# Performance work log

Measured on AMD Instinct MI355X. Metric: run time of the kernel, lower is better.

## Reference

```python
import jax, jax.numpy as jnp
import numpy as np
from jax import lax

LN_EPS = 1e-5

def _layer_norm(x, g, b):
    mu = jnp.mean(x, axis=-1, keepdims=True)
    var = jnp.mean(jnp.square(x - mu), axis=-1, keepdims=True)
    return (x - mu) * lax.rsqrt(var + LN_EPS) * g + b

def _conv1d_same(x, w, b):
    # x: [B, T, Cin], w: [K, Cin, Cout] (kernel=3, padding=1 == SAME)
    y = lax.conv_general_dilated(x, w, window_strides=(1,), padding='SAME',
                                 dimension_numbers=('NWC', 'WIO', 'NWC'))
    return y + b

def setup_inputs() -> dict:
    key = jax.random.key(0)
    ks = jax.random.split(key, 8)
    B, T_enc, D, F = 16, 512, 256, 256
    x = jax.random.normal(ks[0], (B, T_enc, D), dtype=jnp.float32)
    target = jax.random.randint(ks[1], (B, T_enc), 0, 8).astype(jnp.int32)
    s = 0.05
    w1 = jax.random.normal(ks[2], (3, D, F), dtype=jnp.float32) * s
    w2 = jax.random.normal(ks[3], (3, F, F), dtype=jnp.float32) * s
    wl = jax.random.normal(ks[4], (F, 1), dtype=jnp.float32) * s
    return {
        'x': x, 'target': target,
        'w1': w1, 'b1': jnp.zeros((F,), jnp.float32),
        'g1': jnp.ones((F,), jnp.float32), 'be1': jnp.zeros((F,), jnp.float32),
        'w2': w2, 'b2': jnp.zeros((F,), jnp.float32),
        'g2': jnp.ones((F,), jnp.float32), 'be2': jnp.zeros((F,), jnp.float32),
        'wl': wl, 'bl': jnp.zeros((1,), jnp.float32),
        'mel_max_length': 4096,
    }

def reference(x, target, w1, b1, g1, be1, w2, b2, g2, be2, wl, bl, mel_max_length):
    # --- DurationPredictor (eval mode, dropout off) ---
    h = jax.nn.relu(_layer_norm(_conv1d_same(x, w1, b1), g1, be1))
    h = jax.nn.relu(_layer_norm(_conv1d_same(h, w2, b2), g2, be2))
    duration_predictor_output = jnp.exp(h @ wl + bl)[..., 0]  # [B, T_enc]
    # --- LR with ground-truth target durations (training branch) ---
    # alignment[b, t, j] = 1 iff cumsum(target)[b, j-1] <= t < cumsum(target)[b, j]
    cum = jnp.cumsum(target, axis=1)                      # [B, T_enc]
    t = jnp.arange(mel_max_length, dtype=target.dtype)    # [T_mel]
    temp = cum[:, None, :] - t[None, :, None]             # [B, T_mel, T_enc]
    pos = temp > 0
    cond2 = (target[:, None, :] - jnp.where(pos, temp, 0)) >= 0
    alignment = (pos & cond2).astype(x.dtype)             # rows past sum are all-zero => built-in padding
    output = jnp.einsum('bme,bed->bmd', alignment, x)     # [B, T_mel, D]
    return output, alignment, duration_predictor_output
```

## Files before the change

### kernel.cpp

```cpp
#include <hip/hip_runtime.h>

typedef __attribute__((ext_vector_type(8))) short short8;
typedef __attribute__((ext_vector_type(4))) float f32x4;

#define NB   16
#define TENC 512
#define DCH  256
#define TMEL 4096
#define ROWS (NB*TENC)

__device__ __forceinline__ unsigned short f2bf(float f){
  unsigned u = __builtin_bit_cast(unsigned, f);
  u += 0x7FFFu + ((u >> 16) & 1u);
  return (unsigned short)(u >> 16);
}

__global__ __launch_bounds__(256) void prep_scan_kernel(
    const float* __restrict__ x, const int* __restrict__ target,
    const float* __restrict__ w1, const float* __restrict__ w2,
    unsigned* __restrict__ xb32,
    unsigned short* __restrict__ w1p, unsigned short* __restrict__ w2p,
    int* __restrict__ cum, int* __restrict__ total, int* __restrict__ src){
  __shared__ int wsum[4];
  __shared__ int stot;
  int bid = blockIdx.x, tid = threadIdx.x;
  if (bid < 16){
    int lane = tid & 63, wv = tid >> 6;
    int a0 = target[bid * 512 + 2 * tid];
    int a1 = target[bid * 512 + 2 * tid + 1];
    int ps = a0 + a1;
    #pragma unroll
    for (int off = 1; off < 64; off <<= 1){
      int v = __shfl_up(ps, off);
      if (lane >= off) ps += v;
    }
    if (lane == 63) wsum[wv] = ps;
    __syncthreads();
    int add = 0;
    #pragma unroll
    for (int w = 0; w < 4; ++w){ int s = wsum[w]; if (w < wv) add += s; }
    ps += add;
    int c1 = ps;
    int c0 = ps - a1;
    int cp = c0 - a0;
    cum[bid * 512 + 2 * tid]     = c0;
    cum[bid * 512 + 2 * tid + 1] = c1;
    if (tid == 255){ total[bid] = c1; stot = c1; }
    int* sb = src + bid * TMEL;
    for (int t = cp; t < c0; ++t) sb[t] = 2 * tid;
    for (int t = c0; t < c1; ++t) sb[t] = 2 * tid + 1;
    __syncthreads();
    for (int t = stot + tid; t < TMEL; t += 256) sb[t] = -1;
  } else if (bid < 16 + 2048){
    int i = (bid - 16) * 256 + tid;
    const f32x4 v = *reinterpret_cast<const f32x4*>(x + 4 * (size_t)i);
    unsigned lo = (unsigned)f2bf(v.x) | ((unsigned)f2bf(v.y) << 16);
    unsigned hi = (unsigned)f2bf(v.z) | ((unsigned)f2bf(v.w) << 16);
    xb32[2 * i]     = lo;
    xb32[2 * i + 1] = hi;
  } else {
    int i = (bid - 16 - 2048) * 256 + tid;
    int j = i & 7, lane = (i >> 3) & 63, nt = (i >> 9) & 15, ks = i >> 13;
    int r   = ks * 32 + ((lane >> 4) * 8) + j;
    int col = nt * 16 + (lane & 15);
    w1p[i] = f2bf(w1[r * 256 + col]);
    w2p[i] = f2bf(w2[r * 256 + col]);
  }
}

__global__ __launch_bounds__(256, 4) void fused_kernel(
    const float* __restrict__ x, const int* __restrict__ src,
    const unsigned short* __restrict__ xb,
    const unsigned short* __restrict__ w1p, const unsigned short* __restrict__ w2p,
    const float* __restrict__ b1, const float* __restrict__ g1, const float* __restrict__ be1,
    const float* __restrict__ b2, const float* __restrict__ g2, const float* __restrict__ be2,
    const float* __restrict__ wl, const float* __restrict__ bl,
    float* __restrict__ out0, float* __restrict__ alignp, float* __restrict__ durp)
{
  __shared__ unsigned short hsw[48 * 256];
  __shared__ float red[48][4][2];
  __shared__ float dred[16][4];
  int tid = threadIdx.x;

  if (blockIdx.x >= 512){
    int row  = (blockIdx.x - 512) * 4 + (tid >> 6);
    int lane = tid & 63;
    int b = row >> 12;
    int s = __builtin_amdgcn_readfirstlane(src[row]);
    size_t orow = (size_t)row * 256;
    size_t arow = (size_t)row * 512;
    f32x4 z = {0.f, 0.f, 0.f, 0.f};
    if (s < 0){
      *reinterpret_cast<f32x4*>(out0 + orow + lane * 4) = z;
      *reinterpret_cast<f32x4*>(alignp + arow + lane * 8) = z;
      *reinterpret_cast<f32x4*>(alignp + arow + lane * 8 + 4) = z;
      return;
    }
    const f32x4 v = *reinterpret_cast<const f32x4*>(x + ((size_t)b * TENC + s) * DCH + lane * 4);
    *reinterpret_cast<f32x4*>(out0 + orow + lane * 4) = v;
    f32x4 a0 = z, a1 = z;
    int rel = s - lane * 8;
    if (rel >= 0 && rel < 8){
      if (rel < 4) a0[rel] = 1.0f; else a1[rel - 4] = 1.0f;
    }
    *reinterpret_cast<f32x4*>(alignp + arow + lane * 8) = a0;
    *reinterpret_cast<f32x4*>(alignp + arow + lane * 8 + 4) = a1;
    return;
  }

  int m0 = blockIdx.x * 16;
  int rowlo = (m0 >> 9) << 9, rowhi = rowlo + 512;
  int wave = tid >> 6, l = tid & 63, kgrp = l >> 4, l16 = l & 15;
  int colb = wave * 64 + l16;

  f32x4 acc[3][4];
  #pragma unroll
  for (int mt = 0; mt < 3; ++mt)
    #pragma unroll
    for (int nt = 0; nt < 4; ++nt) acc[mt][nt] = (f32x4)0.0f;

  for (int ks = 0; ks < 24; ++ks){
    int shift = ks >> 3;
    int c = (ks & 7) * 32 + kgrp * 8;
    const unsigned short* wb = w1p + (size_t)(ks * 16 + wave * 4) * 512 + l * 8;
    short8 bf0 = *reinterpret_cast<const short8*>(wb);
    short8 bf1 = *reinterpret_cast<const short8*>(wb + 512);
    short8 bf2 = *reinterpret_cast<const short8*>(wb + 1024);
    short8 bf3 = *reinterpret_cast<const short8*>(wb + 1536);
    #pragma unroll
    for (int mt = 0; mt < 3; ++mt){
      int grow = m0 - 16 + mt * 16 + l16 + shift - 1;
      short8 a = {0,0,0,0,0,0,0,0};
      if (grow >= rowlo && grow < rowhi)
        a = *reinterpret_cast<const short8*>(xb + (size_t)grow * 256 + c);
      acc[mt][0] = __builtin_amdgcn_mfma_f32_16x16x32_bf16(a, bf0, acc[mt][0], 0, 0, 0);
      acc[mt][1] = __builtin_amdgcn_mfma_f32_16x16x32_bf16(a, bf1, acc[mt][1], 0, 0, 0);
      acc[mt][2] = __builtin_amdgcn_mfma_f32_16x16x32_bf16(a, bf2, acc[mt][2], 0, 0, 0);
      acc[mt][3] = __builtin_amdgcn_mfma_f32_16x16x32_bf16(a, bf3, acc[mt][3], 0, 0, 0);
    }
  }
  #pragma unroll
  for (int mt = 0; mt < 3; ++mt){
    float s1[4] = {0,0,0,0}, s2[4] = {0,0,0,0};
    #pragma unroll
    for (int nt = 0; nt < 4; ++nt){
      float bv = b1[colb + nt * 16];
      #pragma unroll
      for (int q = 0; q < 4; ++q){
        float v = acc[mt][nt][q] + bv;
        acc[mt][nt][q] = v;
        s1[q] += v; s2[q] += v * v;
      }
    }
    #pragma unroll
    for (int m = 1; m < 16; m <<= 1)
      #pragma unroll
      for (int q = 0; q < 4; ++q){
        s1[q] += __shfl_xor(s1[q], m);
        s2[q] += __shfl_xor(s2[q], m);
      }
    if (l16 == 0)
      #pragma unroll
      for (int q = 0; q < 4; ++q){
        red[mt * 16 + kgrp * 4 + q][wave][0] = s1[q];
        red[mt * 16 + kgrp * 4 + q][wave][1] = s2[q];
      }
  }
  __syncthreads();
  float mu[3][4], rs[3][4];
  #pragma unroll
  for (int mt = 0; mt < 3; ++mt)
    #pragma unroll
    for (int q = 0; q < 4; ++q){
      int r = mt * 16 + kgrp * 4 + q;
      float S1 = red[r][0][0] + red[r][1][0] + red[r][2][0] + red[r][3][0];
      float S2 = red[r][0][1] + red[r][1][1] + red[r][2][1] + red[r][3][1];
      float m_ = S1 * (1.0f / 256.0f);
      float var = S2 * (1.0f / 256.0f) - m_ * m_;
      mu[mt][q] = m_;
      rs[mt][q] = rsqrtf(var + 1e-5f);
    }
  #pragma unroll
  for (int mt = 0; mt < 3; ++mt)
    #pragma unroll
    for (int nt = 0; nt < 4; ++nt){
      int col = colb + nt * 16;
      float g = g1[col], be = be1[col];
      #pragma unroll
      for (int q = 0; q < 4; ++q){
        int r = mt * 16 + kgrp * 4 + q;
        int gq = m0 - 16 + r;
        float y = fmaxf((acc[mt][nt][q] - mu[mt][q]) * rs[mt][q] * g + be, 0.0f);
        unsigned short hv = (gq >= rowlo && gq < rowhi) ? f2bf(y) : (unsigned short)0;
        hsw[r * 256 + (col ^ ((r & 7) << 3))] = hv;
      }
    }
  __syncthreads();

  f32x4 acc2[4];
  #pragma unroll
  for (int nt = 0; nt < 4; ++nt) acc2[nt] = (f32x4)0.0f;

  for (int ks = 0; ks < 24; ++ks){
    int shift = ks >> 3;
    int c = (ks & 7) * 32 + kgrp * 8;
    const unsigned short* wb = w2p + (size_t)(ks * 16 + wave * 4) * 512 + l * 8;
    short8 bf0 = *reinterpret_cast<const short8*>(wb);
    short8 bf1 = *reinterpret_cast<const short8*>(wb + 512);
    short8 bf2 = *reinterpret_cast<const short8*>(wb + 1024);
    short8 bf3 = *reinterpret_cast<const short8*>(wb + 1536);
    int rr = 16 + l16 + shift - 1;
    short8 a = *reinterpret_cast<const short8*>(hsw + rr * 256 + (c ^ ((rr & 7) << 3)));
    acc2[0] = __builtin_amdgcn_mfma_f32_16x16x32_bf16(a, bf0, acc2[0], 0, 0, 0);
    acc2[1] = __builtin_amdgcn_mfma_f32_16x16x32_bf16(a, bf1, acc2[1], 0, 0, 0);
    acc2[2] = __builtin_amdgcn_mfma_f32_16x16x32_bf16(a, bf2, acc2[2], 0, 0, 0);
    acc2[3] = __builtin_amdgcn_mfma_f32_16x16x32_bf16(a, bf3, acc2[3], 0, 0, 0);
  }
  __syncthreads();
  {
    float s1[4] = {0,0,0,0}, s2[4] = {0,0,0,0};
    #pragma unroll
    for (int nt = 0; nt < 4; ++nt){
      float bv = b2[colb + nt * 16];
      #pragma unroll
      for (int q = 0; q < 4; ++q){
        float v = acc2[nt][q] + bv;
        acc2[nt][q] = v;
        s1[q] += v; s2[q] += v * v;
      }
    }
    #pragma unroll
    for (int m = 1; m < 16; m <<= 1)
      #pragma unroll
      for (int q = 0; q < 4; ++q){
        s1[q] += __shfl_xor(s1[q], m);
        s2[q] += __shfl_xor(s2[q], m);
      }
    if (l16 == 0)
      #pragma unroll
      for (int q = 0; q < 4; ++q){
        red[kgrp * 4 + q][wave][0] = s1[q];
        red[kgrp * 4 + q][wave][1] = s2[q];
      }
  }
  __syncthreads();
  {
    float mu2[4], rs2[4];
    #pragma unroll
    for (int q = 0; q < 4; ++q){
      int r = kgrp * 4 + q;
      float S1 = red[r][0][0] + red[r][1][0] + red[r][2][0] + red[r][3][0];
      float S2 = red[r][0][1] + red[r][1][1] + red[r][2][1] + red[r][3][1];
      float m_ = S1 * (1.0f / 256.0f);
      float var = S2 * (1.0f / 256.0f) - m_ * m_;
      mu2[q] = m_;
      rs2[q] = rsqrtf(var + 1e-5f);
    }
    float dp[4] = {0,0,0,0};
    #pragma unroll
    for (int nt = 0; nt < 4; ++nt){
      int col = colb + nt * 16;
      float g = g2[col], be = be2[col], wv = wl[col];
      #pragma unroll
      for (int q = 0; q < 4; ++q){
        float y = fmaxf((acc2[nt][q] - mu2[q]) * rs2[q] * g + be, 0.0f);
        dp[q] += y * wv;
      }
    }
    #pragma unroll
    for (int m = 1; m < 16; m <<= 1)
      #pragma unroll
      for (int q = 0; q < 4; ++q) dp[q] += __shfl_xor(dp[q], m);
    if (l16 == 0)
      #pragma unroll
      for (int q = 0; q < 4; ++q) dred[kgrp * 4 + q][wave] = dp[q];
  }
  __syncthreads();
  if (tid < 16)
    durp[m0 + tid] = expf(dred[tid][0] + dred[tid][1] + dred[tid][2] + dred[tid][3] + bl[0]);
}

extern "C" void kernel_launch(void* const* d_in, const int* in_sizes, int n_in,
                              void* d_out, int out_size, void* d_ws, size_t ws_size,
                              hipStream_t stream){
  const float* x   = (const float*)d_in[0];
  const int*   target = (const int*)d_in[1];
  const float* w1  = (const float*)d_in[2];
  const float* b1  = (const float*)d_in[3];
  const float* g1  = (const float*)d_in[4];
  const float* be1 = (const float*)d_in[5];
  const float* w2  = (const float*)d_in[6];
  const float* b2  = (const float*)d_in[7];
  const float* g2  = (const float*)d_in[8];
  const float* be2 = (const float*)d_in[9];
  const float* wl  = (const float*)d_in[10];
  const float* bl  = (const float*)d_in[11];

  float* out0   = (float*)d_out;
  float* alignp = out0 + (size_t)NB * TMEL * DCH;
  float* durp   = alignp + (size_t)NB * TMEL * TENC;

  char* ws = (char*)d_ws;
  int* cum   = (int*)ws;
  int* total = (int*)(ws + 32768);
  int* src   = (int*)(ws + 65536);
  unsigned short* xb  = (unsigned short*)(ws + 65536 + 262144);
  unsigned short* w1p = (unsigned short*)(ws + 65536 + 262144 + 4194304);
  unsigned short* w2p = (unsigned short*)(ws + 65536 + 262144 + 4194304 + 393216);

  prep_scan_kernel<<<2832, 256, 0, stream>>>(x, target, w1, w2,
      (unsigned*)xb, w1p, w2p, cum, total, src);
  fused_kernel<<<512 + NB * TMEL / 4, 256, 0, stream>>>(x, src, xb, w1p, w2p,
      b1, g1, be1, b2, g2, be2, wl, bl, out0, alignp, durp);
}
```

Measured before the change: 65.05 us.

## Fuse x bf16 conversion into conv kernel via swizzled LDS halo tile

```diff
diff --git a/kernel.cpp b/kernel.cpp
--- a/kernel.cpp
+++ b/kernel.cpp
@@ -2,6 +2,7 @@
 
 typedef __attribute__((ext_vector_type(8))) short short8;
 typedef __attribute__((ext_vector_type(4))) float f32x4;
+typedef __attribute__((ext_vector_type(2))) unsigned u32x2;
 
 #define NB   16
 #define TENC 512
@@ -16,11 +17,10 @@
 }
 
 __global__ __launch_bounds__(256) void prep_scan_kernel(
-    const float* __restrict__ x, const int* __restrict__ target,
+    const int* __restrict__ target,
     const float* __restrict__ w1, const float* __restrict__ w2,
-    unsigned* __restrict__ xb32,
     unsigned short* __restrict__ w1p, unsigned short* __restrict__ w2p,
-    int* __restrict__ cum, int* __restrict__ total, int* __restrict__ src){
+    int* __restrict__ src){
   __shared__ int wsum[4];
   __shared__ int stot;
   int bid = blockIdx.x, tid = threadIdx.x;
@@ -43,42 +43,34 @@
     int c1 = ps;
     int c0 = ps - a1;
     int cp = c0 - a0;
-    cum[bid * 512 + 2 * tid]     = c0;
-    cum[bid * 512 + 2 * tid + 1] = c1;
-    if (tid == 255){ total[bid] = c1; stot = c1; }
+    if (tid == 255) stot = c1;
     int* sb = src + bid * TMEL;
     for (int t = cp; t < c0; ++t) sb[t] = 2 * tid;
     for (int t = c0; t < c1; ++t) sb[t] = 2 * tid + 1;
     __syncthreads();
     for (int t = stot + tid; t < TMEL; t += 256) sb[t] = -1;
-  } else if (bid < 16 + 2048){
+  } else {
     int i = (bid - 16) * 256 + tid;
-    const f32x4 v = *reinterpret_cast<const f32x4*>(x + 4 * (size_t)i);
-    unsigned lo = (unsigned)f2bf(v.x) | ((unsigned)f2bf(v.y) << 16);
-    unsigned hi = (unsigned)f2bf(v.z) | ((unsigned)f2bf(v.w) << 16);
-    xb32[2 * i]     = lo;
-    xb32[2 * i + 1] = hi;
-  } else {
-    int i = (bid - 16 - 2048) * 256 + tid;
-    int j = i & 7, lane = (i >> 3) & 63, nt = (i >> 9) & 15, ks = i >> 13;
-    int r   = ks * 32 + ((lane >> 4) * 8) + j;
-    int col = nt * 16 + (lane & 15);
-    w1p[i] = f2bf(w1[r * 256 + col]);
-    w2p[i] = f2bf(w2[r * 256 + col]);
+    int r = i >> 8, col = i & 255;
+    int ks = r >> 5, rh = (r >> 3) & 3, j = r & 7;
+    int nt = col >> 4, lane = rh * 16 + (col & 15);
+    int o = (((ks << 4) + nt) << 9) + (lane << 3) + j;
+    w1p[o] = f2bf(w1[i]);
+    w2p[o] = f2bf(w2[i]);
   }
 }
 
 __global__ __launch_bounds__(256, 4) void fused_kernel(
     const float* __restrict__ x, const int* __restrict__ src,
-    const unsigned short* __restrict__ xb,
     const unsigned short* __restrict__ w1p, const unsigned short* __restrict__ w2p,
     const float* __restrict__ b1, const float* __restrict__ g1, const float* __restrict__ be1,
     const float* __restrict__ b2, const float* __restrict__ g2, const float* __restrict__ be2,
     const float* __restrict__ wl, const float* __restrict__ bl,
     float* __restrict__ out0, float* __restrict__ alignp, float* __restrict__ durp)
 {
-  __shared__ unsigned short hsw[48 * 256];
-  __shared__ float red[48][4][2];
+  __shared__ unsigned short xsw[34 * 256];
+  __shared__ unsigned short hsw[32 * 256];
+  __shared__ float red[32][4][2];
   __shared__ float dred[16][4];
   int tid = threadIdx.x;
 
@@ -113,9 +105,29 @@
   int wave = tid >> 6, l = tid & 63, kgrp = l >> 4, l16 = l & 15;
   int colb = wave * 64 + l16;
 
-  f32x4 acc[3][4];
-  #pragma unroll
-  for (int mt = 0; mt < 3; ++mt)
+  {
+    int lane = l;
+    #pragma unroll
+    for (int it = 0; it < 9; ++it){
+      int rr = it * 4 + wave;
+      if (rr < 34){
+        int grow = m0 - 2 + rr;
+        f32x4 v = {0.f, 0.f, 0.f, 0.f};
+        if (grow >= rowlo && grow < rowhi)
+          v = *reinterpret_cast<const f32x4*>(x + (size_t)grow * 256 + lane * 4);
+        unsigned lo = (unsigned)f2bf(v.x) | ((unsigned)f2bf(v.y) << 16);
+        unsigned hi = (unsigned)f2bf(v.z) | ((unsigned)f2bf(v.w) << 16);
+        int col = lane * 4;
+        u32x2 pk = {lo, hi};
+        *reinterpret_cast<u32x2*>(xsw + rr * 256 + (col ^ ((rr & 7) << 3))) = pk;
+      }
+    }
+  }
+  __syncthreads();
+
+  f32x4 acc[2][4];
+  #pragma unroll
+  for (int mt = 0; mt < 2; ++mt)
     #pragma unroll
     for (int nt = 0; nt < 4; ++nt) acc[mt][nt] = (f32x4)0.0f;
 
@@ -128,11 +140,9 @@
     short8 bf2 = *reinterpret_cast<const short8*>(wb + 1024);
     short8 bf3 = *reinterpret_cast<const short8*>(wb + 1536);
     #pragma unroll
-    for (int mt = 0; mt < 3; ++mt){
-      int grow = m0 - 16 + mt * 16 + l16 + shift - 1;
-      short8 a = {0,0,0,0,0,0,0,0};
-      if (grow >= rowlo && grow < rowhi)
-        a = *reinterpret_cast<const short8*>(xb + (size_t)grow * 256 + c);
+    for (int mt = 0; mt < 2; ++mt){
+      int rr = mt * 16 + l16 + shift;
+      short8 a = *reinterpret_cast<const short8*>(xsw + rr * 256 + (c ^ ((rr & 7) << 3)));
       acc[mt][0] = __builtin_amdgcn_mfma_f32_16x16x32_bf16(a, bf0, acc[mt][0], 0, 0, 0);
       acc[mt][1] = __builtin_amdgcn_mfma_f32_16x16x32_bf16(a, bf1, acc[mt][1], 0, 0, 0);
       acc[mt][2] = __builtin_amdgcn_mfma_f32_16x16x32_bf16(a, bf2, acc[mt][2], 0, 0, 0);
@@ -140,7 +150,7 @@
     }
   }
   #pragma unroll
-  for (int mt = 0; mt < 3; ++mt){
+  for (int mt = 0; mt < 2; ++mt){
     float s1[4] = {0,0,0,0}, s2[4] = {0,0,0,0};
     #pragma unroll
     for (int nt = 0; nt < 4; ++nt){
@@ -167,9 +177,9 @@
       }
   }
   __syncthreads();
-  float mu[3][4], rs[3][4];
-  #pragma unroll
-  for (int mt = 0; mt < 3; ++mt)
+  float mu[2][4], rs[2][4];
+  #pragma unroll
+  for (int mt = 0; mt < 2; ++mt)
     #pragma unroll
     for (int q = 0; q < 4; ++q){
       int r = mt * 16 + kgrp * 4 + q;
@@ -181,7 +191,7 @@
       rs[mt][q] = rsqrtf(var + 1e-5f);
     }
   #pragma unroll
-  for (int mt = 0; mt < 3; ++mt)
+  for (int mt = 0; mt < 2; ++mt)
     #pragma unroll
     for (int nt = 0; nt < 4; ++nt){
       int col = colb + nt * 16;
@@ -189,7 +199,7 @@
       #pragma unroll
       for (int q = 0; q < 4; ++q){
         int r = mt * 16 + kgrp * 4 + q;
-        int gq = m0 - 16 + r;
+        int gq = m0 - 1 + r;
         float y = fmaxf((acc[mt][nt][q] - mu[mt][q]) * rs[mt][q] * g + be, 0.0f);
         unsigned short hv = (gq >= rowlo && gq < rowhi) ? f2bf(y) : (unsigned short)0;
         hsw[r * 256 + (col ^ ((r & 7) << 3))] = hv;
@@ -209,7 +219,7 @@
     short8 bf1 = *reinterpret_cast<const short8*>(wb + 512);
     short8 bf2 = *reinterpret_cast<const short8*>(wb + 1024);
     short8 bf3 = *reinterpret_cast<const short8*>(wb + 1536);
-    int rr = 16 + l16 + shift - 1;
+    int rr = l16 + shift;
     short8 a = *reinterpret_cast<const short8*>(hsw + rr * 256 + (c ^ ((rr & 7) << 3)));
     acc2[0] = __builtin_amdgcn_mfma_f32_16x16x32_bf16(a, bf0, acc2[0], 0, 0, 0);
     acc2[1] = __builtin_amdgcn_mfma_f32_16x16x32_bf16(a, bf1, acc2[1], 0, 0, 0);
@@ -301,15 +311,11 @@
   float* durp   = alignp + (size_t)NB * TMEL * TENC;
 
   char* ws = (char*)d_ws;
-  int* cum   = (int*)ws;
-  int* total = (int*)(ws + 32768);
-  int* src   = (int*)(ws + 65536);
-  unsigned short* xb  = (unsigned short*)(ws + 65536 + 262144);
-  unsigned short* w1p = (unsigned short*)(ws + 65536 + 262144 + 4194304);
-  unsigned short* w2p = (unsigned short*)(ws + 65536 + 262144 + 4194304 + 393216);
-
-  prep_scan_kernel<<<2832, 256, 0, stream>>>(x, target, w1, w2,
-      (unsigned*)xb, w1p, w2p, cum, total, src);
-  fused_kernel<<<512 + NB * TMEL / 4, 256, 0, stream>>>(x, src, xb, w1p, w2p,
+  int* src = (int*)ws;
+  unsigned short* w1p = (unsigned short*)(ws + 262144);
+  unsigned short* w2p = (unsigned short*)(ws + 262144 + 393216);
+
+  prep_scan_kernel<<<784, 256, 0, stream>>>(target, w1, w2, w1p, w2p, src);
+  fused_kernel<<<512 + NB * TMEL / 4, 256, 0, stream>>>(x, src, w1p, w2p,
       b1, g1, be1, b2, g2, be2, wl, bl, out0, alignp, durp);
 }
```

New measurement: 52.72 us (median of 2 runs). 1.23x faster.
